# Performance work log

Measured on AMD Instinct MI355X. Metric: run time of the kernel, lower is better.

Reference implementation:

```python
import jax, jax.numpy as jnp
import numpy as np


def setup_inputs() -> dict:
    key = jax.random.key(0)
    ks = jax.random.split(key, 7)
    N, H, W, C, O, K, WD, NW = 16, 64, 64, 512, 512, 3, 512, 14
    return {
        "x": jax.random.normal(ks[0], (N, H, W, C), jnp.float32),
        "dlatents": jax.random.normal(ks[1], (N, NW, WD), jnp.float32),
        "style_w": jax.random.normal(ks[2], (WD, C), jnp.float32),
        "style_b": jnp.ones((C,), jnp.float32),          # bias_init=1 in LinearLayer
        "weight": jax.random.normal(ks[3], (K, K, C, O), jnp.float32),
        "bias": jax.random.normal(ks[4], (O,), jnp.float32) * 0.1,
        "noise_strength": jax.random.normal(ks[5], (), jnp.float32) * 0.1,
        "noise": jax.random.normal(ks[6], (N, H, W, 1), jnp.float32),
        "layer_idx": 7,
    }


def reference(x, dlatents, style_w, style_b, weight, bias, noise_strength, noise, layer_idx):
    N, H, W, C = x.shape
    K = weight.shape[0]
    w_dim = dlatents.shape[-1]
    # Style linear with equalized learning rate (he_std = 1/sqrt(in), lr_multiplier = 1)
    dl = dlatents[:, layer_idx]                               # [N, w_dim]
    s = dl @ (style_w * (1.0 / np.sqrt(w_dim))) + style_b     # [N, C] per-sample styles
    # Equalized-lr conv weight
    w = weight * (1.0 / np.sqrt(K * K * C))                   # [K, K, C, O]
    # Demodulation coeffs d[n,o] = rsqrt(sum_{k,k,i} (w*s)^2 + eps), computed
    # without materializing the per-sample [N,K,K,C,O] modulated weights.
    d = jax.lax.rsqrt(jnp.einsum('hwio,ni->no', jnp.square(w), jnp.square(s)) + 1e-8)  # [N, O]
    # Non-fused modulated conv: scale inputs, shared-weight conv, scale outputs.
    y = jax.lax.conv_general_dilated(
        x * s[:, None, None, :], w,
        window_strides=(1, 1), padding='SAME',
        dimension_numbers=('NHWC', 'HWIO', 'NHWC'))           # [N, H, W, O]
    y = y * d[:, None, None, :]
    # Noise injection + bias + activation (leaky_relu with gain sqrt(2))
    y = y + noise * noise_strength
    y = y + bias
    return jax.nn.leaky_relu(y, 0.2) * np.sqrt(2.0)
```

## Files before the change

### kernel.cpp

```cpp
#include <hip/hip_runtime.h>
#include <hip/hip_bf16.h>

typedef __attribute__((ext_vector_type(8))) short bf16x8;
typedef __attribute__((ext_vector_type(4))) float f32x4;
typedef __attribute__((ext_vector_type(8))) short shortx8;

#define WBT_OFF_B 71368704ull
#define S_OFF_B   76087296ull
#define D_OFF_B   76120064ull
#define W2_OFF_B  76152832ull

__device__ __forceinline__ void gload16(const void* g, void* l) {
  __builtin_amdgcn_global_load_lds((const __attribute__((address_space(1))) void*)g,
                                   (__attribute__((address_space(3))) void*)l, 16, 0, 0);
}

__global__ void style_kernel(const float* __restrict__ dlat, const float* __restrict__ sw,
                             const float* __restrict__ sb, const int* __restrict__ lidx,
                             float* __restrict__ s) {
  int gid = blockIdx.x * 256 + threadIdx.x;
  int n = gid >> 9, c = gid & 511;
  const float* dl = dlat + (n * 14 + lidx[0]) * 512;
  float acc = 0.f;
  for (int k = 0; k < 512; ++k) acc = fmaf(dl[k], sw[k * 512 + c], acc);
  s[gid] = acc * 0.044194173824159216f + sb[c];
}

__global__ void w2_kernel(const float* __restrict__ weight, float* __restrict__ w2) {
  int gid = blockIdx.x * 256 + threadIdx.x;
  int i = gid >> 9, o = gid & 511;
  float acc = 0.f;
#pragma unroll
  for (int t = 0; t < 9; ++t) { float v = weight[(t * 512 + i) * 512 + o]; acc = fmaf(v, v, acc); }
  w2[gid] = acc;
}

__global__ void d_kernel(const float* __restrict__ w2, const float* __restrict__ s,
                         float* __restrict__ dd) {
  int gid = blockIdx.x * 256 + threadIdx.x;
  int n = gid >> 9, o = gid & 511;
  const float* sn = s + (n << 9);
  float acc = 0.f;
  for (int i = 0; i < 512; ++i) { float sv = sn[i]; acc = fmaf(w2[(i << 9) + o], sv * sv, acc); }
  dd[gid] = rsqrtf(acc * (1.0f / 4608.0f) + 1e-8f);
}

__global__ void wbt_kernel(const float* __restrict__ weight, __hip_bfloat16* __restrict__ wbT) {
  int gid = blockIdx.x * 256 + threadIdx.x;
  int i = gid & 511, o = (gid >> 9) & 511, t = gid >> 18;
  float v = weight[(t * 512 + i) * 512 + o] * 0.014731391274719739f;
  wbT[gid] = __float2bfloat16(v);
}

__global__ void xpad_kernel(const float* __restrict__ x, const float* __restrict__ s,
                            __hip_bfloat16* __restrict__ xsp) {
  int gid = blockIdx.x * 256 + threadIdx.x;
  int c8 = gid & 63;
  int pos = gid >> 6;
  int wp = pos % 66; int t1 = pos / 66; int hp = t1 % 66; int n = t1 / 66;
  shortx8 ov;
  if ((unsigned)(hp - 1) < 64u && (unsigned)(wp - 1) < 64u) {
    const float* xp = &x[((((n << 6) + (hp - 1)) << 6) + (wp - 1)) * 512 + (c8 << 3)];
    const float* sp = &s[(n << 9) + (c8 << 3)];
    float4 a0 = *(const float4*)xp, a1 = *(const float4*)(xp + 4);
    float4 s0 = *(const float4*)sp, s1 = *(const float4*)(sp + 4);
    float r[8] = {a0.x * s0.x, a0.y * s0.y, a0.z * s0.z, a0.w * s0.w,
                  a1.x * s1.x, a1.y * s1.y, a1.z * s1.z, a1.w * s1.w};
#pragma unroll
    for (int j = 0; j < 8; ++j) { __hip_bfloat16 h = __float2bfloat16(r[j]); ov[j] = *(short*)&h; }
  } else {
#pragma unroll
    for (int j = 0; j < 8; ++j) ov[j] = 0;
  }
  *(shortx8*)&xsp[(size_t)pos * 512 + (c8 << 3)] = ov;
}

__global__ void conv_kernel(const __hip_bfloat16* __restrict__ xsp,
                            const __hip_bfloat16* __restrict__ wbT,
                            const float* __restrict__ dbuf,
                            const float* __restrict__ bias,
                            const float* __restrict__ noise,
                            const float* __restrict__ nstr,
                            float* __restrict__ out) {
  __shared__ short Ald[128 * 32];
  __shared__ short Bld[128 * 32];

  int bid = blockIdx.x;
  bid = (bid & 7) * 256 + (bid >> 3);
  int mTile = bid >> 2, nTile = bid & 3;

  int tid = threadIdx.x;
  int lane = tid & 63, wv = tid >> 6;
  int wm = wv >> 1, wn = wv & 1;

  int m_base = mTile << 7;
  int n_img = m_base >> 12;
  int h_b = (m_base & 4095) >> 6;
  int oB = nTile << 7;

  int rlow = (wv << 4) + (lane >> 2);
  int seg = (lane & 3) << 3;

  int xb0 = ((n_img * 66 + h_b) * 66 + rlow) * 512 + seg;
  int xb1 = ((n_img * 66 + h_b + 1) * 66 + rlow) * 512 + seg;
  int bb0 = (oB + rlow) * 512 + seg;
  int bb1 = (oB + 64 + rlow) * 512 + seg;

  short* la0 = &Ald[wv * 512];
  short* la1 = &Ald[(4 + wv) * 512];
  short* lb0 = &Bld[wv * 512];
  short* lb1 = &Bld[(4 + wv) * 512];

  int arow = (wm << 6) + (lane & 15);
  int brow = (wn << 6) + (lane & 15);
  int koff = (lane >> 4) << 3;

  f32x4 acc[4][4];
#pragma unroll
  for (int f = 0; f < 4; ++f)
#pragma unroll
    for (int g = 0; g < 4; ++g) acc[f][g] = {0.f, 0.f, 0.f, 0.f};

#pragma unroll 1
  for (int tap = 0; tap < 9; ++tap) {
    int toff = ((tap / 3) * 66 + (tap % 3)) * 512;
    const __hip_bfloat16* ga0 = xsp + xb0 + toff;
    const __hip_bfloat16* ga1 = xsp + xb1 + toff;
    const __hip_bfloat16* gb0 = wbT + tap * 262144 + bb0;
    const __hip_bfloat16* gb1 = wbT + tap * 262144 + bb1;
#pragma unroll 1
    for (int kb = 0; kb < 16; ++kb) {
      __syncthreads();
      gload16(ga0, la0); gload16(ga1, la1);
      gload16(gb0, lb0); gload16(gb1, lb1);
      __syncthreads();
      ga0 += 32; ga1 += 32; gb0 += 32; gb1 += 32;
      bf16x8 af[4], bfr[4];
#pragma unroll
      for (int f = 0; f < 4; ++f) af[f] = *(const bf16x8*)&Ald[(arow + (f << 4)) * 32 + koff];
#pragma unroll
      for (int g = 0; g < 4; ++g) bfr[g] = *(const bf16x8*)&Bld[(brow + (g << 4)) * 32 + koff];
#pragma unroll
      for (int f = 0; f < 4; ++f)
#pragma unroll
        for (int g = 0; g < 4; ++g)
          acc[f][g] = __builtin_amdgcn_mfma_f32_16x16x32_bf16(af[f], bfr[g], acc[f][g], 0, 0, 0);
    }
  }

  float ns = nstr[0];
  int ocol = oB + (wn << 6) + (lane & 15);
  float dv[4], bv[4];
#pragma unroll
  for (int g = 0; g < 4; ++g) {
    dv[g] = dbuf[(n_img << 9) + ocol + (g << 4)];
    bv[g] = bias[ocol + (g << 4)];
  }
  int mrow0 = m_base + (wm << 6) + ((lane >> 4) << 2);
#pragma unroll
  for (int f = 0; f < 4; ++f) {
#pragma unroll
    for (int j = 0; j < 4; ++j) {
      int m = mrow0 + (f << 4) + j;
      float nz = noise[m] * ns;
      float* op = out + (size_t)m * 512 + ocol;
#pragma unroll
      for (int g = 0; g < 4; ++g) {
        float v = fmaf(acc[f][g][j], dv[g], nz + bv[g]);
        v = (v > 0.f ? v : 0.2f * v) * 1.4142135623730951f;
        op[g << 4] = v;
      }
    }
  }
}

extern "C" void kernel_launch(void* const* d_in, const int* in_sizes, int n_in,
                              void* d_out, int out_size, void* d_ws, size_t ws_size,
                              hipStream_t stream) {
  const float* x     = (const float*)d_in[0];
  const float* dlat  = (const float*)d_in[1];
  const float* sw    = (const float*)d_in[2];
  const float* sb    = (const float*)d_in[3];
  const float* wt    = (const float*)d_in[4];
  const float* bias  = (const float*)d_in[5];
  const float* nstr  = (const float*)d_in[6];
  const float* noise = (const float*)d_in[7];
  const int*   lidx  = (const int*)d_in[8];
  float* out = (float*)d_out;

  char* ws = (char*)d_ws;
  __hip_bfloat16* xsp = (__hip_bfloat16*)ws;
  __hip_bfloat16* wbT = (__hip_bfloat16*)(ws + WBT_OFF_B);
  float* sbuf = (float*)(ws + S_OFF_B);
  float* dbuf = (float*)(ws + D_OFF_B);
  float* w2   = (float*)(ws + W2_OFF_B);

  style_kernel<<<32, 256, 0, stream>>>(dlat, sw, sb, lidx, sbuf);
  w2_kernel<<<1024, 256, 0, stream>>>(wt, w2);
  d_kernel<<<32, 256, 0, stream>>>(w2, sbuf, dbuf);
  wbt_kernel<<<9216, 256, 0, stream>>>(wt, wbT);
  xpad_kernel<<<17424, 256, 0, stream>>>(x, sbuf, xsp);
  conv_kernel<<<2048, 256, 0, stream>>>(xsp, wbT, dbuf, bias, noise, nstr, out);
}
```

Measured before the change: 643.7 us.

## Tile weight transpose through LDS and split demod reduction with atomics

```diff
diff --git a/kernel.cpp b/kernel.cpp
--- a/kernel.cpp
+++ b/kernel.cpp
@@ -22,6 +22,7 @@
   int n = gid >> 9, c = gid & 511;
   const float* dl = dlat + (n * 14 + lidx[0]) * 512;
   float acc = 0.f;
+#pragma unroll 4
   for (int k = 0; k < 512; ++k) acc = fmaf(dl[k], sw[k * 512 + c], acc);
   s[gid] = acc * 0.044194173824159216f + sb[c];
 }
@@ -35,21 +36,44 @@
   w2[gid] = acc;
 }
 
-__global__ void d_kernel(const float* __restrict__ w2, const float* __restrict__ s,
-                         float* __restrict__ dd) {
-  int gid = blockIdx.x * 256 + threadIdx.x;
-  int n = gid >> 9, o = gid & 511;
-  const float* sn = s + (n << 9);
+__global__ void dpart_kernel(const float* __restrict__ w2, const float* __restrict__ s,
+                             float* __restrict__ dpre) {
+  int b = blockIdx.x;
+  int n = b >> 3, ic = (b >> 1) & 3, oh = b & 1;
+  int o = (oh << 8) + threadIdx.x;
+  const float* sn = s + (n << 9) + (ic << 7);
+  const float* w2p = w2 + ((ic << 7) << 9) + o;
   float acc = 0.f;
-  for (int i = 0; i < 512; ++i) { float sv = sn[i]; acc = fmaf(w2[(i << 9) + o], sv * sv, acc); }
-  dd[gid] = rsqrtf(acc * (1.0f / 4608.0f) + 1e-8f);
+#pragma unroll 4
+  for (int i = 0; i < 128; ++i) { float sv = sn[i]; acc = fmaf(w2p[i << 9], sv * sv, acc); }
+  atomicAdd(&dpre[(n << 9) + o], acc);
 }
 
 __global__ void wbt_kernel(const float* __restrict__ weight, __hip_bfloat16* __restrict__ wbT) {
-  int gid = blockIdx.x * 256 + threadIdx.x;
-  int i = gid & 511, o = (gid >> 9) & 511, t = gid >> 18;
-  float v = weight[(t * 512 + i) * 512 + o] * 0.014731391274719739f;
-  wbT[gid] = __float2bfloat16(v);
+  __shared__ float tile[64][65];
+  int b = blockIdx.x;
+  int t = b >> 6; int rem = b & 63;
+  int i0 = (rem >> 3) << 6, o0 = (rem & 7) << 6;
+  int tr = threadIdx.x >> 4;
+  int tc = (threadIdx.x & 15) << 2;
+#pragma unroll
+  for (int rr = 0; rr < 4; ++rr) {
+    int il = tr + (rr << 4);
+    float4 v = *(const float4*)&weight[((size_t)(t * 512 + i0 + il) << 9) + o0 + tc];
+    tile[il][tc] = v.x; tile[il][tc + 1] = v.y; tile[il][tc + 2] = v.z; tile[il][tc + 3] = v.w;
+  }
+  __syncthreads();
+#pragma unroll
+  for (int rr = 0; rr < 4; ++rr) {
+    int ol = tr + (rr << 4);
+    short4 ov;
+#pragma unroll
+    for (int j = 0; j < 4; ++j) {
+      __hip_bfloat16 h = __float2bfloat16(tile[tc + j][ol] * 0.014731391274719739f);
+      ((short*)&ov)[j] = *(short*)&h;
+    }
+    *(short4*)&wbT[((size_t)(t * 512 + o0 + ol) << 9) + i0 + tc] = ov;
+  }
 }
 
 __global__ void xpad_kernel(const float* __restrict__ x, const float* __restrict__ s,
@@ -77,7 +101,7 @@
 
 __global__ void conv_kernel(const __hip_bfloat16* __restrict__ xsp,
                             const __hip_bfloat16* __restrict__ wbT,
-                            const float* __restrict__ dbuf,
+                            const float* __restrict__ dpre,
                             const float* __restrict__ bias,
                             const float* __restrict__ noise,
                             const float* __restrict__ nstr,
@@ -153,7 +177,7 @@
   float dv[4], bv[4];
 #pragma unroll
   for (int g = 0; g < 4; ++g) {
-    dv[g] = dbuf[(n_img << 9) + ocol + (g << 4)];
+    dv[g] = rsqrtf(dpre[(n_img << 9) + ocol + (g << 4)] * (1.0f / 4608.0f) + 1e-8f);
     bv[g] = bias[ocol + (g << 4)];
   }
   int mrow0 = m_base + (wm << 6) + ((lane >> 4) << 2);
@@ -192,13 +216,14 @@
   __hip_bfloat16* xsp = (__hip_bfloat16*)ws;
   __hip_bfloat16* wbT = (__hip_bfloat16*)(ws + WBT_OFF_B);
   float* sbuf = (float*)(ws + S_OFF_B);
-  float* dbuf = (float*)(ws + D_OFF_B);
+  float* dpre = (float*)(ws + D_OFF_B);
   float* w2   = (float*)(ws + W2_OFF_B);
 
+  hipMemsetAsync(dpre, 0, 16 * 512 * sizeof(float), stream);
   style_kernel<<<32, 256, 0, stream>>>(dlat, sw, sb, lidx, sbuf);
   w2_kernel<<<1024, 256, 0, stream>>>(wt, w2);
-  d_kernel<<<32, 256, 0, stream>>>(w2, sbuf, dbuf);
-  wbt_kernel<<<9216, 256, 0, stream>>>(wt, wbT);
+  dpart_kernel<<<128, 256, 0, stream>>>(w2, sbuf, dpre);
+  wbt_kernel<<<576, 256, 0, stream>>>(wt, wbT);
   xpad_kernel<<<17424, 256, 0, stream>>>(x, sbuf, xsp);
-  conv_kernel<<<2048, 256, 0, stream>>>(xsp, wbT, dbuf, bias, noise, nstr, out);
-}
+  conv_kernel<<<2048, 256, 0, stream>>>(xsp, wbT, dpre, bias, noise, nstr, out);
+}
```

New measurement: 641.2 us. No clear change (-0.4%).
